# Kernel optimization log

Measured on AMD Instinct MI355X. Metric: run time of the kernel, lower is better.

## Reference

```python
import jax, jax.numpy as jnp
import numpy as np

T, B, D, H = 512, 128, 1024, 1024

def setup_inputs() -> dict:
    key = jax.random.key(0)
    ks = jax.random.split(key, 5)
    stdv = 1.0 / np.sqrt(H)
    u = lambda k, shape: jax.random.uniform(k, shape, jnp.float32, -stdv, stdv)
    return {
        "x": jax.random.normal(ks[0], (T, B, D), jnp.float32),
        "w_ih": u(ks[1], (4 * H, D)),
        "b_ih": u(ks[2], (4 * H,)),
        "w_hh": u(ks[3], (4 * H, H)),
        "b_hh": u(ks[4], (4 * H,)),
    }

def _lstm(x, w_ih, b_ih, w_hh, b_hh):
    # Precompute input projections for all timesteps in one big GEMM: [T,B,4H]
    gx = jnp.einsum('tbd,gd->tbg', x, w_ih) + b_ih + b_hh
    h0 = jnp.zeros((x.shape[1], H), x.dtype)
    c0 = jnp.zeros((x.shape[1], H), x.dtype)

    def step(carry, gx_t):
        h_prev, c_prev = carry
        gates = gx_t + h_prev @ w_hh.T  # [B,4H]
        i_t, f_t, g_t, o_t = jnp.split(gates, 4, axis=1)
        i_t = jax.nn.sigmoid(i_t)
        f_t = jax.nn.sigmoid(f_t)
        g_t = jnp.tanh(g_t)
        o_t = jax.nn.sigmoid(o_t)
        c_t = f_t * c_prev + i_t * g_t
        h_t = o_t * jnp.tanh(c_t)
        return (h_t, c_t), h_t

    (h_n, c_n), hs = jax.lax.scan(step, (h0, c0), gx)
    return hs, (h_n, c_n)

def reference(x, w_ih, b_ih, w_hh, b_hh):
    # Returns (output [T,B,H], (h_n [B,H], c_n [B,H])) matching DPLSTM.forward
    out, (h_n, c_n) = _lstm(x, w_ih, b_ih, w_hh, b_hh)
    return out, (h_n, c_n)
```

## Files before the change

kernel.cpp:

```cpp
#include <hip/hip_runtime.h>
#include <hip/hip_bf16.h>


#define NT 512
#define NB 128
#define ND 1024
#define NH 1024
#define FSTR 16
#define GX_BLK 16384
#define GX_SLOT (32 * GX_BLK)
#define GUARD_STEP (1 << 17)
#define GUARD_BOOT (1 << 22)

typedef __attribute__((ext_vector_type(8))) __bf16 bf16x8;
typedef __attribute__((ext_vector_type(4))) float  f32x4;
typedef __attribute__((ext_vector_type(2))) unsigned long long ullx2;
typedef unsigned long long u64;

__device__ __forceinline__ float sigm(float x) { return 1.0f / (1.0f + __expf(-x)); }
__device__ __forceinline__ float tanh_(float x) {
    x = fminf(15.0f, fmaxf(-15.0f, x));
    float e = __expf(-2.0f * x);
    return (1.0f - e) / (1.0f + e);
}
__device__ __forceinline__ bf16x8 cvt8v(float4 f0, float4 f1) {
    bf16x8 v;
    v[0] = (__bf16)f0.x; v[1] = (__bf16)f0.y; v[2] = (__bf16)f0.z; v[3] = (__bf16)f0.w;
    v[4] = (__bf16)f1.x; v[5] = (__bf16)f1.y; v[6] = (__bf16)f1.z; v[7] = (__bf16)f1.w;
    return v;
}
__device__ __forceinline__ bf16x8 cvt8(const float* p) {
    return cvt8v(*(const float4*)p, *(const float4*)(p + 4));
}
__device__ __forceinline__ u64 ald(const u64* p) {
    return __hip_atomic_load(p, __ATOMIC_RELAXED, __HIP_MEMORY_SCOPE_AGENT);
}
__device__ __forceinline__ void ast(u64* p, u64 v) {
    __hip_atomic_store(p, v, __ATOMIC_RELAXED, __HIP_MEMORY_SCOPE_AGENT);
}
__device__ __forceinline__ unsigned aldu(const unsigned* p) {
    return __hip_atomic_load(p, __ATOMIC_RELAXED, __HIP_MEMORY_SCOPE_AGENT);
}
__device__ __forceinline__ void astu(unsigned* p, unsigned v) {
    __hip_atomic_store(p, v, __ATOMIC_RELAXED, __HIP_MEMORY_SCOPE_AGENT);
}

__global__ void __launch_bounds__(512, 2)
lstm_main(const float* __restrict__ x, const float* __restrict__ w_ih,
          const float* __restrict__ b_ih, const float* __restrict__ w_hh,
          const float* __restrict__ b_hh, float* __restrict__ out,
          float* __restrict__ gxr,
          unsigned* __restrict__ hbuf,
          unsigned* __restrict__ l3f,
          unsigned* __restrict__ xfl)
{
    __shared__ uint4 ldsA[4096];
    __shared__ float scr[8][32][17];

    const int tid  = threadIdx.x;
    const int lane = tid & 63;
    const int wid  = tid >> 6;
    const int bid  = blockIdx.x;
    const int c = lane & 15, kslot = lane >> 4;

    if (bid < 128) {
        const int g = bid >> 5, blk = bid & 31;

        bf16x8 wreg[32];
        {
            const size_t grow = (size_t)(c >> 2) * NH + blk * 32 + 4 * wid + (c & 3);
            const float* wp = w_hh + grow * NH + kslot * 8;
            #pragma unroll
            for (int kk = 0; kk < 32; ++kk) wreg[kk] = cvt8(wp + kk * 32);
        }
        const int row_l = lane >> 1;
        const int jjo   = (lane & 1) * 2;
        const int j0    = blk * 32 + 4 * wid + jjo;
        float bias[4][2];
        #pragma unroll
        for (int gg = 0; gg < 4; ++gg)
            #pragma unroll
            for (int u = 0; u < 2; ++u)
                bias[gg][u] = b_ih[gg * NH + j0 + u] + b_hh[gg * NH + j0 + u];
        float cst[2] = {0.f, 0.f};

        unsigned* postl3 = l3f + ((size_t)g * 32 + blk) * FSTR;

        f32x4 gxc0, gxc1;
        #define GXLOAD(sl) do {                                                      \
            const u64* gp_ = (const u64*)(const void*)gxr                            \
                + ((((size_t)(sl)) * 32 + blk) * GX_BLK                              \
                   + (size_t)(wid * 16 + c) * 128 + 32 * g + kslot * 4) / 2;         \
            const u64 q0_ = ald(gp_), q1_ = ald(gp_ + 1);                            \
            const u64 q2_ = ald(gp_ + 8), q3_ = ald(gp_ + 9);                        \
            ullx2 t0_, t1_;                                                          \
            t0_[0] = q0_; t0_[1] = q1_; t1_[0] = q2_; t1_[1] = q3_;                  \
            gxc0 = __builtin_bit_cast(f32x4, t0_);                                   \
            gxc1 = __builtin_bit_cast(f32x4, t1_);                                   \
        } while (0)

        {
            const unsigned* xfp0 = xfl + ((size_t)blk * 4 + 0) * FSTR;
            int gu = 0;
            while (aldu(xfp0) < 1u) {
                __builtin_amdgcn_s_sleep(8);
                if (++gu > GUARD_BOOT) break;
            }
            GXLOAD(0);
        }

        for (int t = 0; t < NT; ++t) {
            if (t) {
                if (tid < 32) {
                    const unsigned* f = l3f + ((size_t)g * 32 + tid) * FSTR;
                    int gu = 0;
                    while (aldu(f) < (unsigned)t) {
                        __builtin_amdgcn_s_sleep(1);
                        if (++gu > GUARD_STEP) break;
                    }
                }
                __syncthreads();
                const u64* s8 = (const u64*)(const void*)
                    (hbuf + ((size_t)g * 2 + ((t + 1) & 1)) * 16384);
                u64 st[16];
                #pragma unroll
                for (int i = 0; i < 8; ++i) {
                    const size_t q = (size_t)(i * 512 + tid) * 2;
                    st[2 * i]     = ald(s8 + q);
                    st[2 * i + 1] = ald(s8 + q + 1);
                }
                #pragma unroll
                for (int i = 0; i < 8; ++i) {
                    ullx2 tq; tq[0] = st[2 * i]; tq[1] = st[2 * i + 1];
                    ldsA[i * 512 + tid] = __builtin_bit_cast(uint4, tq);
                }
            }
            const unsigned* xfp = xfl + ((size_t)blk * 4 + ((t + 1) & 3)) * FSTR;
            unsigned xfNext = 0xffffffffu;
            if (t + 1 < NT) xfNext = aldu(xfp);
            __syncthreads();

            f32x4 acc0, acc1;
            if (t) {
                f32x4 a0a = gxc0, a1a = gxc1;
                f32x4 a0b = {0,0,0,0}, a1b = {0,0,0,0};
                #pragma unroll
                for (int kk = 0; kk < 32; ++kk) {
                    const bf16x8 a0 = __builtin_bit_cast(bf16x8, ldsA[(kk*4 + kslot)*32 + c]);
                    const bf16x8 a1 = __builtin_bit_cast(bf16x8, ldsA[(kk*4 + kslot)*32 + 16 + c]);
                    if (kk & 1) {
                        a0b = __builtin_amdgcn_mfma_f32_16x16x32_bf16(a0, wreg[kk], a0b, 0,0,0);
                        a1b = __builtin_amdgcn_mfma_f32_16x16x32_bf16(a1, wreg[kk], a1b, 0,0,0);
                    } else {
                        a0a = __builtin_amdgcn_mfma_f32_16x16x32_bf16(a0, wreg[kk], a0a, 0,0,0);
                        a1a = __builtin_amdgcn_mfma_f32_16x16x32_bf16(a1, wreg[kk], a1a, 0,0,0);
                    }
                }
                acc0 = a0a + a0b; acc1 = a1a + a1b;
            } else {
                acc0 = gxc0; acc1 = gxc1;
            }

            #pragma unroll
            for (int r = 0; r < 4; ++r) {
                scr[wid][kslot * 4 + r][c]      = acc0[r];
                scr[wid][16 + kslot * 4 + r][c] = acc1[r];
            }
            float hv[2];
            #pragma unroll
            for (int u = 0; u < 2; ++u) {
                const float iv = sigm (scr[wid][row_l][ 0 + jjo + u] + bias[0][u]);
                const float fv = sigm (scr[wid][row_l][ 4 + jjo + u] + bias[1][u]);
                const float gv = tanh_(scr[wid][row_l][ 8 + jjo + u] + bias[2][u]);
                const float ov = sigm (scr[wid][row_l][12 + jjo + u] + bias[3][u]);
                const float cc = fv * cst[u] + iv * gv;
                cst[u] = cc;
                hv[u] = ov * tanh_(cc);
            }

            {
                const unsigned short u0 = __builtin_bit_cast(unsigned short, (__bf16)hv[0]);
                const unsigned short u1 = __builtin_bit_cast(unsigned short, (__bf16)hv[1]);
                const unsigned pack = (unsigned)u0 | ((unsigned)u1 << 16);
                const size_t hidx = ((size_t)g * 2 + (t & 1)) * 16384
                                  + ((size_t)(j0 >> 3) * 32 + row_l) * 4 + ((j0 & 7) >> 1);
                astu(&hbuf[hidx], pack);
            }
            __syncthreads();
            if (tid == 0) astu(postl3, (unsigned)(t + 1));

            {
                float2 o; o.x = hv[0]; o.y = hv[1];
                *(float2*)&out[((size_t)t * NB + 32 * g + row_l) * NH + j0] = o;
                if (t == NT - 1)
                    *(float2*)&out[(size_t)NT * NB * NH + ((size_t)32 * g + row_l) * NH + j0] = o;
            }
            if (t + 1 < NT) {
                int gu = 0;
                while (xfNext < (unsigned)(t + 2)) {
                    __builtin_amdgcn_s_sleep(1);
                    xfNext = aldu(xfp);
                    if (++gu > GUARD_STEP) break;
                }
                GXLOAD((t + 1) & 3);
            }
        }
        {
            float2 cn; cn.x = cst[0]; cn.y = cst[1];
            *(float2*)&out[(size_t)NT * NB * NH + (size_t)NB * NH
                           + ((size_t)32 * g + row_l) * NH + j0] = cn;
        }
    } else {
        const int e = (bid - 128) >> 5, r = bid & 31;

        bf16x8 wreg[32];
        {
            const size_t grow = (size_t)(c >> 2) * NH + r * 32 + 4 * wid + (c & 3);
            const float* wp = w_ih + grow * ND + kslot * 8;
            #pragma unroll
            for (int kk = 0; kk < 32; ++kk) wreg[kk] = cvt8(wp + kk * 32);
        }
        const int xrow = tid >> 4, seg = tid & 15;

        for (int tt = e; tt < NT; tt += 4) {
            if (tt >= 4) {
                const unsigned* hp = l3f + ((size_t)(lane & 3) * 32 + r) * FSTR;
                int gu = 0;
                while (aldu(hp) < (unsigned)(tt - 3)) {
                    __builtin_amdgcn_s_sleep(4);
                    if (++gu > GUARD_STEP) break;
                }
            }
            __syncthreads();

            f32x4 xa0={0,0,0,0}, xa1={0,0,0,0}, xa2={0,0,0,0}, xa3={0,0,0,0};
            f32x4 xa4={0,0,0,0}, xa5={0,0,0,0}, xa6={0,0,0,0}, xa7={0,0,0,0};

            #define XCHUNK(m, A, B) {                                                \
                const float* xs = x + ((size_t)tt * NB + 32 * (m) + xrow) * ND       \
                                    + seg * 64;                                      \
                float4 xf[16];                                                       \
                _Pragma("unroll")                                                    \
                for (int i2 = 0; i2 < 8; ++i2) {                                     \
                    xf[2 * i2]     = *(const float4*)(xs + i2 * 8);                  \
                    xf[2 * i2 + 1] = *(const float4*)(xs + i2 * 8 + 4);              \
                }                                                                    \
                _Pragma("unroll")                                                    \
                for (int i2 = 0; i2 < 8; ++i2)                                       \
                    ldsA[(seg * 8 + i2) * 32 + xrow] =                               \
                        __builtin_bit_cast(uint4, cvt8v(xf[2*i2], xf[2*i2+1]));      \
                __syncthreads();                                                     \
                _Pragma("unroll")                                                    \
                for (int kk = 0; kk < 32; ++kk) {                                    \
                    const bf16x8 a0 = __builtin_bit_cast(bf16x8,                     \
                        ldsA[(kk*4 + kslot)*32 + c]);                                \
                    const bf16x8 a1 = __builtin_bit_cast(bf16x8,                     \
                        ldsA[(kk*4 + kslot)*32 + 16 + c]);                           \
                    A = __builtin_amdgcn_mfma_f32_16x16x32_bf16(a0, wreg[kk], A, 0,0,0);\
                    B = __builtin_amdgcn_mfma_f32_16x16x32_bf16(a1, wreg[kk], B, 0,0,0);\
                }                                                                    \
                __syncthreads(); }

            XCHUNK(0, xa0, xa1)
            XCHUNK(1, xa2, xa3)
            XCHUNK(2, xa4, xa5)
            XCHUNK(3, xa6, xa7)

            {
                u64* gp = (u64*)(void*)gxr
                    + (((size_t)(tt & 3) * 32 + r) * GX_BLK
                       + (size_t)(wid * 16 + c) * 128 + kslot * 4) / 2;
                #define XSTORE(mt, A) {                                              \
                    const ullx2 q_ = __builtin_bit_cast(ullx2, A);                   \
                    ast(gp + (mt) * 8, q_[0]); ast(gp + (mt) * 8 + 1, q_[1]); }
                XSTORE(0, xa0) XSTORE(1, xa1) XSTORE(2, xa2) XSTORE(3, xa3)
                XSTORE(4, xa4) XSTORE(5, xa5) XSTORE(6, xa6) XSTORE(7, xa7)
            }
            __syncthreads();
            if (tid == 0)
                astu(xfl + ((size_t)r * 4 + (tt & 3)) * FSTR, (unsigned)(tt + 1));
        }
    }
}

extern "C" void kernel_launch(void* const* d_in, const int* in_sizes, int n_in,
                              void* d_out, int out_size, void* d_ws, size_t ws_size,
                              hipStream_t stream)
{
    const float* x    = (const float*)d_in[0];
    const float* w_ih = (const float*)d_in[1];
    const float* b_ih = (const float*)d_in[2];
    const float* w_hh = (const float*)d_in[3];
    const float* b_hh = (const float*)d_in[4];
    float* out = (float*)d_out;

    const size_t gx_bytes = (size_t)4 * GX_SLOT * sizeof(float);
    const size_t hb_bytes = (size_t)4 * 2 * 16384 * sizeof(unsigned);
    const size_t fl_bytes = (size_t)128 * FSTR * sizeof(unsigned);
    const size_t total    = gx_bytes + hb_bytes + 2 * fl_bytes;
    if (ws_size < total) return;

    char* p = (char*)d_ws;
    float*    gxr  = (float*)p;      p += gx_bytes;
    unsigned* hbuf = (unsigned*)p;   p += hb_bytes;
    unsigned* l3f  = (unsigned*)p;   p += fl_bytes;
    unsigned* xfl  = (unsigned*)p;

    hipMemsetAsync(d_ws, 0, total, stream);

    void* args[] = { (void*)&x, (void*)&w_ih, (void*)&b_ih, (void*)&w_hh,
                     (void*)&b_hh, (void*)&out, (void*)&gxr, (void*)&hbuf,
                     (void*)&l3f, (void*)&xfl };
    hipError_t err = hipLaunchCooperativeKernel((const void*)lstm_main,
                                                dim3(256), dim3(512),
                                                args, 0, stream);
    if (err != hipSuccess) {
        lstm_main<<<dim3(256), dim3(512), 0, stream>>>(x, w_ih, b_ih, w_hh, b_hh,
                                                       out, gxr, hbuf, l3f, xfl);
    }
}
```

Measured before the change: 4.486 ms.

## Store gx in bf16 and use a 32-deep h ring with cached loads

Input-projection results are now packed to bf16 before they go to the workspace, which halves the gx traffic, and they are unpacked back to fp32 on load. The hidden-state exchange buffer becomes a 32-slot ring when the workspace allows it. Blocks can then read h with ordinary cached 128-bit loads instead of relaxed atomic loads, with an acquire fence every 32 steps to invalidate stale cache lines. This trades gx precision (bf16 rounding of the input projection) for bandwidth, and depends on the fence cadence being enough for cache coherence across slots. The spin sleep is also raised slightly.

```diff
diff --git a/kernel.cpp b/kernel.cpp
--- a/kernel.cpp
+++ b/kernel.cpp
@@ -7,8 +7,6 @@
 #define ND 1024
 #define NH 1024
 #define FSTR 16
-#define GX_BLK 16384
-#define GX_SLOT (32 * GX_BLK)
 #define GUARD_STEP (1 << 17)
 #define GUARD_BOOT (1 << 22)
 
@@ -44,15 +42,26 @@
 __device__ __forceinline__ void astu(unsigned* p, unsigned v) {
     __hip_atomic_store(p, v, __ATOMIC_RELAXED, __HIP_MEMORY_SCOPE_AGENT);
 }
+__device__ __forceinline__ float b2f(unsigned bits16) {
+    return __builtin_bit_cast(float, bits16 << 16);
+}
+__device__ __forceinline__ u64 pack4(f32x4 v) {
+    const unsigned short h0 = __builtin_bit_cast(unsigned short, (__bf16)v[0]);
+    const unsigned short h1 = __builtin_bit_cast(unsigned short, (__bf16)v[1]);
+    const unsigned short h2 = __builtin_bit_cast(unsigned short, (__bf16)v[2]);
+    const unsigned short h3 = __builtin_bit_cast(unsigned short, (__bf16)v[3]);
+    return (u64)h0 | ((u64)h1 << 16) | ((u64)h2 << 32) | ((u64)h3 << 48);
+}
 
 __global__ void __launch_bounds__(512, 2)
 lstm_main(const float* __restrict__ x, const float* __restrict__ w_ih,
           const float* __restrict__ b_ih, const float* __restrict__ w_hh,
           const float* __restrict__ b_hh, float* __restrict__ out,
-          float* __restrict__ gxr,
+          u64* __restrict__ gxr,
           unsigned* __restrict__ hbuf,
           unsigned* __restrict__ l3f,
-          unsigned* __restrict__ xfl)
+          unsigned* __restrict__ xfl,
+          int hmask, int cached)
 {
     __shared__ uint4 ldsA[4096];
     __shared__ float scr[8][32][17];
@@ -88,15 +97,18 @@
 
         f32x4 gxc0, gxc1;
         #define GXLOAD(sl) do {                                                      \
-            const u64* gp_ = (const u64*)(const void*)gxr                            \
-                + ((((size_t)(sl)) * 32 + blk) * GX_BLK                              \
-                   + (size_t)(wid * 16 + c) * 128 + 32 * g + kslot * 4) / 2;         \
-            const u64 q0_ = ald(gp_), q1_ = ald(gp_ + 1);                            \
-            const u64 q2_ = ald(gp_ + 8), q3_ = ald(gp_ + 9);                        \
-            ullx2 t0_, t1_;                                                          \
-            t0_[0] = q0_; t0_[1] = q1_; t1_[0] = q2_; t1_[1] = q3_;                  \
-            gxc0 = __builtin_bit_cast(f32x4, t0_);                                   \
-            gxc1 = __builtin_bit_cast(f32x4, t1_);                                   \
+            const u64* gp_ = gxr + (((size_t)(sl)) * 32 + blk) * 4096                \
+                             + (size_t)(wid * 16 + c) * 32 + 8 * g;                  \
+            const u64 q0_ = ald(gp_ + kslot);                                        \
+            const u64 q1_ = ald(gp_ + 4 + kslot);                                    \
+            gxc0[0] = b2f((unsigned)q0_ & 0xffffu);                                  \
+            gxc0[1] = b2f(((unsigned)q0_) >> 16);                                    \
+            gxc0[2] = b2f((unsigned)(q0_ >> 32) & 0xffffu);                          \
+            gxc0[3] = b2f((unsigned)(q0_ >> 48));                                    \
+            gxc1[0] = b2f((unsigned)q1_ & 0xffffu);                                  \
+            gxc1[1] = b2f(((unsigned)q1_) >> 16);                                    \
+            gxc1[2] = b2f((unsigned)(q1_ >> 32) & 0xffffu);                          \
+            gxc1[3] = b2f((unsigned)(q1_ >> 48));                                    \
         } while (0)
 
         {
@@ -110,29 +122,42 @@
         }
 
         for (int t = 0; t < NT; ++t) {
+            if (cached && (t & 31) == 0) {
+                if (tid < 64) __builtin_amdgcn_fence(__ATOMIC_ACQUIRE, "agent");
+                __syncthreads();
+            }
             if (t) {
                 if (tid < 32) {
                     const unsigned* f = l3f + ((size_t)g * 32 + tid) * FSTR;
                     int gu = 0;
                     while (aldu(f) < (unsigned)t) {
-                        __builtin_amdgcn_s_sleep(1);
+                        __builtin_amdgcn_s_sleep(2);
                         if (++gu > GUARD_STEP) break;
                     }
                 }
                 __syncthreads();
-                const u64* s8 = (const u64*)(const void*)
-                    (hbuf + ((size_t)g * 2 + ((t + 1) & 1)) * 16384);
-                u64 st[16];
-                #pragma unroll
-                for (int i = 0; i < 8; ++i) {
-                    const size_t q = (size_t)(i * 512 + tid) * 2;
-                    st[2 * i]     = ald(s8 + q);
-                    st[2 * i + 1] = ald(s8 + q + 1);
-                }
-                #pragma unroll
-                for (int i = 0; i < 8; ++i) {
-                    ullx2 tq; tq[0] = st[2 * i]; tq[1] = st[2 * i + 1];
-                    ldsA[i * 512 + tid] = __builtin_bit_cast(uint4, tq);
+                const size_t hbase = ((size_t)((t - 1) & hmask) * 4 + g) * 16384;
+                if (cached) {
+                    const uint4* s4 = (const uint4*)(const void*)(hbuf + hbase);
+                    uint4 stc[8];
+                    #pragma unroll
+                    for (int i = 0; i < 8; ++i) stc[i] = s4[i * 512 + tid];
+                    #pragma unroll
+                    for (int i = 0; i < 8; ++i) ldsA[i * 512 + tid] = stc[i];
+                } else {
+                    const u64* s8 = (const u64*)(const void*)(hbuf + hbase);
+                    u64 st[16];
+                    #pragma unroll
+                    for (int i = 0; i < 8; ++i) {
+                        const size_t q = (size_t)(i * 512 + tid) * 2;
+                        st[2 * i]     = ald(s8 + q);
+                        st[2 * i + 1] = ald(s8 + q + 1);
+                    }
+                    #pragma unroll
+                    for (int i = 0; i < 8; ++i) {
+                        ullx2 tq; tq[0] = st[2 * i]; tq[1] = st[2 * i + 1];
+                        ldsA[i * 512 + tid] = __builtin_bit_cast(uint4, tq);
+                    }
                 }
             }
             const unsigned* xfp = xfl + ((size_t)blk * 4 + ((t + 1) & 3)) * FSTR;
@@ -182,7 +207,7 @@
                 const unsigned short u0 = __builtin_bit_cast(unsigned short, (__bf16)hv[0]);
                 const unsigned short u1 = __builtin_bit_cast(unsigned short, (__bf16)hv[1]);
                 const unsigned pack = (unsigned)u0 | ((unsigned)u1 << 16);
-                const size_t hidx = ((size_t)g * 2 + (t & 1)) * 16384
+                const size_t hidx = ((size_t)(t & hmask) * 4 + g) * 16384
                                   + ((size_t)(j0 >> 3) * 32 + row_l) * 4 + ((j0 & 7) >> 1);
                 astu(&hbuf[hidx], pack);
             }
@@ -267,14 +292,16 @@
             XCHUNK(3, xa6, xa7)
 
             {
-                u64* gp = (u64*)(void*)gxr
-                    + (((size_t)(tt & 3) * 32 + r) * GX_BLK
-                       + (size_t)(wid * 16 + c) * 128 + kslot * 4) / 2;
-                #define XSTORE(mt, A) {                                              \
-                    const ullx2 q_ = __builtin_bit_cast(ullx2, A);                   \
-                    ast(gp + (mt) * 8, q_[0]); ast(gp + (mt) * 8 + 1, q_[1]); }
-                XSTORE(0, xa0) XSTORE(1, xa1) XSTORE(2, xa2) XSTORE(3, xa3)
-                XSTORE(4, xa4) XSTORE(5, xa5) XSTORE(6, xa6) XSTORE(7, xa7)
+                u64* gp = gxr + (((size_t)(tt & 3)) * 32 + r) * 4096
+                          + (size_t)(wid * 16 + c) * 32;
+                ast(gp + kslot,          pack4(xa0));
+                ast(gp + 4 + kslot,      pack4(xa1));
+                ast(gp + 8 + kslot,      pack4(xa2));
+                ast(gp + 12 + kslot,     pack4(xa3));
+                ast(gp + 16 + kslot,     pack4(xa4));
+                ast(gp + 20 + kslot,     pack4(xa5));
+                ast(gp + 24 + kslot,     pack4(xa6));
+                ast(gp + 28 + kslot,     pack4(xa7));
             }
             __syncthreads();
             if (tid == 0)
@@ -294,14 +321,24 @@
     const float* b_hh = (const float*)d_in[4];
     float* out = (float*)d_out;
 
-    const size_t gx_bytes = (size_t)4 * GX_SLOT * sizeof(float);
-    const size_t hb_bytes = (size_t)4 * 2 * 16384 * sizeof(unsigned);
+    const size_t gx_bytes = (size_t)4 * 32 * 4096 * sizeof(u64);
     const size_t fl_bytes = (size_t)128 * FSTR * sizeof(unsigned);
-    const size_t total    = gx_bytes + hb_bytes + 2 * fl_bytes;
-    if (ws_size < total) return;
+    const size_t hb_full  = (size_t)32 * 4 * 16384 * sizeof(unsigned);
+    const size_t hb_min   = (size_t)2  * 4 * 16384 * sizeof(unsigned);
+
+    int hmask, cached;
+    size_t hb_bytes;
+    if (ws_size >= gx_bytes + hb_full + 2 * fl_bytes) {
+        hmask = 31; cached = 1; hb_bytes = hb_full;
+    } else if (ws_size >= gx_bytes + hb_min + 2 * fl_bytes) {
+        hmask = 1;  cached = 0; hb_bytes = hb_min;
+    } else {
+        return;
+    }
+    const size_t total = gx_bytes + hb_bytes + 2 * fl_bytes;
 
     char* p = (char*)d_ws;
-    float*    gxr  = (float*)p;      p += gx_bytes;
+    u64*      gxr  = (u64*)p;        p += gx_bytes;
     unsigned* hbuf = (unsigned*)p;   p += hb_bytes;
     unsigned* l3f  = (unsigned*)p;   p += fl_bytes;
     unsigned* xfl  = (unsigned*)p;
@@ -310,12 +347,13 @@
 
     void* args[] = { (void*)&x, (void*)&w_ih, (void*)&b_ih, (void*)&w_hh,
                      (void*)&b_hh, (void*)&out, (void*)&gxr, (void*)&hbuf,
-                     (void*)&l3f, (void*)&xfl };
+                     (void*)&l3f, (void*)&xfl, (void*)&hmask, (void*)&cached };
     hipError_t err = hipLaunchCooperativeKernel((const void*)lstm_main,
                                                 dim3(256), dim3(512),
                                                 args, 0, stream);
     if (err != hipSuccess) {
         lstm_main<<<dim3(256), dim3(512), 0, stream>>>(x, w_ih, b_ih, w_hh, b_hh,
-                                                       out, gxr, hbuf, l3f, xfl);
+                                                       out, gxr, hbuf, l3f, xfl,
+                                                       hmask, cached);
     }
 }
```

After: 3.944 ms. 12.1% less time.

## Store gate projections in bf16 and replace block barrier with per-wave flag polling

Applied to the files above, without the earlier changes.

The input-projection gate buffer passed between producer and consumer blocks is now stored as packed bf16 instead of fp32, which halves its global traffic. In the recurrent step, each wave polls only the four producer flags whose h slices it copies into LDS, instead of one wave polling all 32 followed by a block-wide barrier. The h loads are remapped so each wave copies exactly those k-slices. Compiler-level fences replace the barrier for ordering. The exchange loses precision on the gate projections, and relying on relaxed atomics with only compiler fences may weaken memory ordering.

```diff
diff --git a/kernel.cpp b/kernel.cpp
--- a/kernel.cpp
+++ b/kernel.cpp
@@ -7,10 +7,11 @@
 #define ND 1024
 #define NH 1024
 #define FSTR 16
-#define GX_BLK 16384
-#define GX_SLOT (32 * GX_BLK)
 #define GUARD_STEP (1 << 17)
 #define GUARD_BOOT (1 << 22)
+
+#define FENCE_ACQ() do { asm volatile("" ::: "memory"); \
+                         __builtin_amdgcn_sched_barrier(0); } while (0)
 
 typedef __attribute__((ext_vector_type(8))) __bf16 bf16x8;
 typedef __attribute__((ext_vector_type(4))) float  f32x4;
@@ -44,12 +45,22 @@
 __device__ __forceinline__ void astu(unsigned* p, unsigned v) {
     __hip_atomic_store(p, v, __ATOMIC_RELAXED, __HIP_MEMORY_SCOPE_AGENT);
 }
+__device__ __forceinline__ float b2f(unsigned bits16) {
+    return __builtin_bit_cast(float, bits16 << 16);
+}
+__device__ __forceinline__ u64 pack4(f32x4 v) {
+    const unsigned short h0 = __builtin_bit_cast(unsigned short, (__bf16)v[0]);
+    const unsigned short h1 = __builtin_bit_cast(unsigned short, (__bf16)v[1]);
+    const unsigned short h2 = __builtin_bit_cast(unsigned short, (__bf16)v[2]);
+    const unsigned short h3 = __builtin_bit_cast(unsigned short, (__bf16)v[3]);
+    return (u64)h0 | ((u64)h1 << 16) | ((u64)h2 << 32) | ((u64)h3 << 48);
+}
 
 __global__ void __launch_bounds__(512, 2)
 lstm_main(const float* __restrict__ x, const float* __restrict__ w_ih,
           const float* __restrict__ b_ih, const float* __restrict__ w_hh,
           const float* __restrict__ b_hh, float* __restrict__ out,
-          float* __restrict__ gxr,
+          u64* __restrict__ gxr,
           unsigned* __restrict__ hbuf,
           unsigned* __restrict__ l3f,
           unsigned* __restrict__ xfl)
@@ -88,15 +99,18 @@
 
         f32x4 gxc0, gxc1;
         #define GXLOAD(sl) do {                                                      \
-            const u64* gp_ = (const u64*)(const void*)gxr                            \
-                + ((((size_t)(sl)) * 32 + blk) * GX_BLK                              \
-                   + (size_t)(wid * 16 + c) * 128 + 32 * g + kslot * 4) / 2;         \
-            const u64 q0_ = ald(gp_), q1_ = ald(gp_ + 1);                            \
-            const u64 q2_ = ald(gp_ + 8), q3_ = ald(gp_ + 9);                        \
-            ullx2 t0_, t1_;                                                          \
-            t0_[0] = q0_; t0_[1] = q1_; t1_[0] = q2_; t1_[1] = q3_;                  \
-            gxc0 = __builtin_bit_cast(f32x4, t0_);                                   \
-            gxc1 = __builtin_bit_cast(f32x4, t1_);                                   \
+            const u64* gp_ = gxr + (((size_t)(sl)) * 32 + blk) * 4096                \
+                             + (size_t)(wid * 16 + c) * 32 + 8 * g;                  \
+            const u64 q0_ = ald(gp_ + kslot);                                        \
+            const u64 q1_ = ald(gp_ + 4 + kslot);                                    \
+            gxc0[0] = b2f((unsigned)q0_ & 0xffffu);                                  \
+            gxc0[1] = b2f(((unsigned)q0_) >> 16);                                    \
+            gxc0[2] = b2f((unsigned)(q0_ >> 32) & 0xffffu);                          \
+            gxc0[3] = b2f((unsigned)(q0_ >> 48));                                    \
+            gxc1[0] = b2f((unsigned)q1_ & 0xffffu);                                  \
+            gxc1[1] = b2f(((unsigned)q1_) >> 16);                                    \
+            gxc1[2] = b2f((unsigned)(q1_ >> 32) & 0xffffu);                          \
+            gxc1[3] = b2f((unsigned)(q1_ >> 48));                                    \
         } while (0)
 
         {
@@ -106,33 +120,44 @@
                 __builtin_amdgcn_s_sleep(8);
                 if (++gu > GUARD_BOOT) break;
             }
+            FENCE_ACQ();
             GXLOAD(0);
         }
 
         for (int t = 0; t < NT; ++t) {
             if (t) {
-                if (tid < 32) {
-                    const unsigned* f = l3f + ((size_t)g * 32 + tid) * FSTR;
+                {
                     int gu = 0;
-                    while (aldu(f) < (unsigned)t) {
+                    for (;;) {
+                        unsigned v = 0xffffffffu;
+                        if (lane < 4)
+                            v = aldu(l3f + ((size_t)g * 32 + 4 * wid + lane) * FSTR);
+                        if (__all(v >= (unsigned)t)) break;
                         __builtin_amdgcn_s_sleep(1);
                         if (++gu > GUARD_STEP) break;
                     }
                 }
-                __syncthreads();
+                FENCE_ACQ();
+
                 const u64* s8 = (const u64*)(const void*)
                     (hbuf + ((size_t)g * 2 + ((t + 1) & 1)) * 16384);
                 u64 st[16];
                 #pragma unroll
                 for (int i = 0; i < 8; ++i) {
-                    const size_t q = (size_t)(i * 512 + tid) * 2;
+                    const int idx = i * 64 + lane;
+                    const int k8  = 16 * wid + (idx >> 5);
+                    const int row = idx & 31;
+                    const size_t q = (size_t)(k8 * 32 + row) * 2;
                     st[2 * i]     = ald(s8 + q);
                     st[2 * i + 1] = ald(s8 + q + 1);
                 }
                 #pragma unroll
                 for (int i = 0; i < 8; ++i) {
+                    const int idx = i * 64 + lane;
+                    const int k8  = 16 * wid + (idx >> 5);
+                    const int row = idx & 31;
                     ullx2 tq; tq[0] = st[2 * i]; tq[1] = st[2 * i + 1];
-                    ldsA[i * 512 + tid] = __builtin_bit_cast(uint4, tq);
+                    ldsA[k8 * 32 + row] = __builtin_bit_cast(uint4, tq);
                 }
             }
             const unsigned* xfp = xfl + ((size_t)blk * 4 + ((t + 1) & 3)) * FSTR;
@@ -202,6 +227,7 @@
                     xfNext = aldu(xfp);
                     if (++gu > GUARD_STEP) break;
                 }
+                FENCE_ACQ();
                 GXLOAD((t + 1) & 3);
             }
         }
@@ -267,14 +293,16 @@
             XCHUNK(3, xa6, xa7)
 
             {
-                u64* gp = (u64*)(void*)gxr
-                    + (((size_t)(tt & 3) * 32 + r) * GX_BLK
-                       + (size_t)(wid * 16 + c) * 128 + kslot * 4) / 2;
-                #define XSTORE(mt, A) {                                              \
-                    const ullx2 q_ = __builtin_bit_cast(ullx2, A);                   \
-                    ast(gp + (mt) * 8, q_[0]); ast(gp + (mt) * 8 + 1, q_[1]); }
-                XSTORE(0, xa0) XSTORE(1, xa1) XSTORE(2, xa2) XSTORE(3, xa3)
-                XSTORE(4, xa4) XSTORE(5, xa5) XSTORE(6, xa6) XSTORE(7, xa7)
+                u64* gp = gxr + (((size_t)(tt & 3)) * 32 + r) * 4096
+                          + (size_t)(wid * 16 + c) * 32;
+                ast(gp + kslot,      pack4(xa0));
+                ast(gp + 4 + kslot,  pack4(xa1));
+                ast(gp + 8 + kslot,  pack4(xa2));
+                ast(gp + 12 + kslot, pack4(xa3));
+                ast(gp + 16 + kslot, pack4(xa4));
+                ast(gp + 20 + kslot, pack4(xa5));
+                ast(gp + 24 + kslot, pack4(xa6));
+                ast(gp + 28 + kslot, pack4(xa7));
             }
             __syncthreads();
             if (tid == 0)
@@ -294,14 +322,14 @@
     const float* b_hh = (const float*)d_in[4];
     float* out = (float*)d_out;
 
-    const size_t gx_bytes = (size_t)4 * GX_SLOT * sizeof(float);
+    const size_t gx_bytes = (size_t)4 * 32 * 4096 * sizeof(u64);
     const size_t hb_bytes = (size_t)4 * 2 * 16384 * sizeof(unsigned);
     const size_t fl_bytes = (size_t)128 * FSTR * sizeof(unsigned);
     const size_t total    = gx_bytes + hb_bytes + 2 * fl_bytes;
     if (ws_size < total) return;
 
     char* p = (char*)d_ws;
-    float*    gxr  = (float*)p;      p += gx_bytes;
+    u64*      gxr  = (u64*)p;        p += gx_bytes;
     unsigned* hbuf = (unsigned*)p;   p += hb_bytes;
     unsigned* l3f  = (unsigned*)p;   p += fl_bytes;
     unsigned* xfl  = (unsigned*)p;
```

Result: faster. 4.113 ms (-8.3%).
